# Kernel tuning notes

Measured on AMD Instinct MI355X. Metric: run time of the kernel, lower is better.

The kernel has to match this reference:

```python
import jax, jax.numpy as jnp
import numpy as np

# ---- hyperparameters (from init_kwargs) ----
SIGMA, RHO = 1.0, 10.0
ALPHA, BETA = 1.0, 1.0
K = 3  # ksize; patches are non-overlapping KxK, structure tensor computed on each patch
GRAY_W = np.array([0.2989, 0.587, 0.114], dtype=np.float32)  # torchvision Grayscale weights


def _gauss1d(sigma):
    d = np.arange(-1.0, 2.0, dtype=np.float32)  # radius-1 kernel (fits 3x3 patches)
    g = np.exp(-d * d / (2.0 * sigma * sigma))
    return (g / g.sum()).astype(np.float32)


def _dgauss1d(sigma):
    d = np.arange(-1.0, 2.0, dtype=np.float32)
    g = _gauss1d(sigma)
    return (-d / (sigma * sigma) * g).astype(np.float32)


def _conv3(x, k2d):
    # 'same' zero-padded 3x3 correlation over the last two dims, fully broadcast
    H, W = x.shape[-2], x.shape[-1]
    xp = jnp.pad(x, [(0, 0)] * (x.ndim - 2) + [(1, 1), (1, 1)])
    out = jnp.zeros_like(x)
    for i in range(3):
        for j in range(3):
            out = out + k2d[i, j] * xp[..., i:i + H, j:j + W]
    return out


# precomputed separable kernels (numpy constants)
_G_S, _DG_S, _G_R = _gauss1d(SIGMA), _dgauss1d(SIGMA), _gauss1d(RHO)
_KX = np.outer(_G_S, _DG_S)   # d/dx (last axis), gaussian-smoothed
_KY = np.outer(_DG_S, _G_S)   # d/dy
_KS = np.outer(_G_R, _G_R)    # rho smoothing


def _structure_tensor(gray):
    # gray: (..., K, K) -> (..., 3, K, K) components (Jxx, Jyy, Jxy)
    Ix = _conv3(gray, _KX)
    Iy = _conv3(gray, _KY)
    Jxx = _conv3(Ix * Ix, _KS)
    Jyy = _conv3(Iy * Iy, _KS)
    Jxy = _conv3(Ix * Iy, _KS)
    return jnp.stack([Jxx, Jyy, Jxy], axis=-3)


def _compute_patches(img):
    # img: (B, 3, H, W) -> (B, P, 3*K*K); non-overlapping KxK patches,
    # grayscale -> structure tensor -> per-patch L2 normalize (vectorized, no vmap-of-tiny-ops)
    B, C, H, W = img.shape
    Hb, Wb = H // K, W // K
    p = img.reshape(B, C, Hb, K, Wb, K).transpose(0, 2, 4, 1, 3, 5)  # (B,Hb,Wb,3,K,K)
    p = p.reshape(B, Hb * Wb, C, K, K)
    gray = jnp.einsum('bpchw,c->bphw', p, jnp.asarray(GRAY_W, p.dtype))
    st = _structure_tensor(gray)                                      # (B,P,3,K,K)
    n = jnp.sqrt(jnp.sum(st * st, axis=(-3, -2, -1), keepdims=True)) + 1e-12
    st = st / n
    return st.reshape(B, Hb * Wb, 3 * K * K)


def _resize(img, factor):
    B, C, H, W = img.shape
    return jax.image.resize(img, (B, C, int(H * factor), int(W * factor)),
                            method='bicubic', antialias=False)


def _pairdist_sq(a, b):
    # squared L2 pairwise distance (monotone in L2; only used for argmin)
    aa = jnp.sum(a * a, axis=-1)[:, :, None]
    bb = jnp.sum(b * b, axis=-1)[:, None, :]
    ab = jnp.einsum('bnw,bmw->bnm', a, b)
    return aa + bb - 2.0 * ab


def _loss(x, gt):
    p1 = _compute_patches(x)
    p2 = _compute_patches(gt)
    p2_2 = _compute_patches(_resize(gt, 0.5))
    p2_4 = _compute_patches(_resize(gt, 0.25))
    p2c = jnp.concatenate([p2, p2_2, p2_4], axis=1)      # (B, P2cat, 27)
    score = ALPHA * _pairdist_sq(p1, p2c) + BETA * _pairdist_sq(p2, p2c)
    ind = jnp.argmin(score, axis=2)                      # (B, P1) nearest-neighbor indices
    sel = jnp.take_along_axis(p2c, ind[:, :, None], axis=1)
    return jnp.mean(jnp.abs(p1 - sel))                   # L1 criterion


def setup_inputs() -> dict:
    key = jax.random.key(0)
    k1, k2 = jax.random.split(key)
    x = jax.random.uniform(k1, (4, 3, 192, 192), dtype=jnp.float32)
    gt = jax.random.uniform(k2, (4, 3, 192, 192), dtype=jnp.float32)
    return {'x': x, 'gt': gt}


def reference(x, gt):
    return _loss(x, gt)
```

## Files before the change

### kernel.cpp

```cpp
#include <hip/hip_runtime.h>
#include <hip/hip_bf16.h>
#include <math.h>

namespace {
constexpr int BATCH = 4;
constexpr int IMG   = 192;
constexpr int PL    = IMG * IMG;
constexpr int NP1   = 4096;
constexpr int N96   = 1024;
constexpr int N48   = 256;
constexpr int MALL  = 5376;
constexpr int RS    = 28;
constexpr int NCHUNK = 16;
constexpr int TPC    = 21;

#define GA 0.27406862f
#define GB 0.45186276f
#define RC 0.33277732f
#define RD 0.33444537f

typedef __bf16 bf16x8 __attribute__((ext_vector_type(8)));
typedef float  f32x4  __attribute__((ext_vector_type(4)));

__device__ __forceinline__ void conv3(const float in[9], const float k[9], float out[9]) {
#pragma unroll
  for (int y = 0; y < 3; ++y)
#pragma unroll
    for (int x = 0; x < 3; ++x) {
      float s = 0.f;
#pragma unroll
      for (int i = 0; i < 3; ++i) {
        int yy = y + i - 1;
        if (yy < 0 || yy > 2) continue;
#pragma unroll
        for (int j = 0; j < 3; ++j) {
          int xx = x + j - 1;
          if (xx < 0 || xx > 2) continue;
          s = fmaf(k[i * 3 + j], in[yy * 3 + xx], s);
        }
      }
      out[y * 3 + x] = s;
    }
}

__device__ __forceinline__ void st_from_gray(const float gray[9], float stv[27], float& cs) {
  const float KX[9] = {GA * GA, 0.f, -GA * GA, GB * GA, 0.f, -GB * GA, GA * GA, 0.f, -GA * GA};
  const float KY[9] = {GA * GA, GA * GB, GA * GA, 0.f, 0.f, 0.f, -GA * GA, -GA * GB, -GA * GA};
  const float KS[9] = {RC * RC, RC * RD, RC * RC, RD * RC, RD * RD, RD * RC, RC * RC, RC * RD, RC * RC};
  float Ix[9], Iy[9];
  conv3(gray, KX, Ix);
  conv3(gray, KY, Iy);
  float Pxx[9], Pyy[9], Pxy[9];
#pragma unroll
  for (int t = 0; t < 9; ++t) {
    Pxx[t] = Ix[t] * Ix[t];
    Pyy[t] = Iy[t] * Iy[t];
    Pxy[t] = Ix[t] * Iy[t];
  }
  conv3(Pxx, KS, stv + 0);
  conv3(Pyy, KS, stv + 9);
  conv3(Pxy, KS, stv + 18);
  float s2 = 0.f;
#pragma unroll
  for (int d = 0; d < 27; ++d) s2 = fmaf(stv[d], stv[d], s2);
  float inv = 1.0f / (sqrtf(s2) + 1e-12f);
  float c = 0.f;
#pragma unroll
  for (int d = 0; d < 27; ++d) {
    stv[d] *= inv;
    c = fmaf(stv[d], stv[d], c);
  }
  cs = c;
}

__device__ __forceinline__ void mkw(int k0, int IS, float w[4], int k[4]) {
  const float W4[4] = {-0.0625f, 0.5625f, 0.5625f, -0.0625f};
  float ssum = 0.f;
#pragma unroll
  for (int u = 0; u < 4; ++u) {
    int kk = k0 + u;
    bool v = (kk >= 0) && (kk < IS);
    w[u] = v ? W4[u] : 0.f;
    k[u] = v ? kk : 0;
    ssum += w[u];
  }
  float inv = 1.f / ssum;
#pragma unroll
  for (int u = 0; u < 4; ++u) w[u] *= inv;
}

__device__ __forceinline__ float bicubic_gray(const float* __restrict__ im,
                                              int i, int j, int step, int koff) {
  float wr[4], wc[4];
  int kr[4], kc[4];
  mkw(step * i + koff, IMG, wr, kr);
  mkw(step * j + koff, IMG, wc, kc);
  float acc = 0.f;
#pragma unroll
  for (int u = 0; u < 4; ++u) {
    float rs = 0.f;
#pragma unroll
    for (int v = 0; v < 4; ++v) {
      int o = kr[u] * IMG + kc[v];
      float r  = im[o];
      float g2 = im[PL + o];
      float bl = im[2 * PL + o];
      float gy = fmaf(0.114f, bl, fmaf(0.587f, g2, 0.2989f * r));
      rs = fmaf(wc[v], gy, rs);
    }
    acc = fmaf(wr[u], rs, acc);
  }
  return acc;
}

__device__ __forceinline__ void pack_row(const float v[28], unsigned* __restrict__ dst) {
  unsigned uh[16], ul[16];
#pragma unroll
  for (int p = 0; p < 16; ++p) {
    float a  = (2 * p < 28) ? v[2 * p] : 0.f;
    float bb = (2 * p + 1 < 28) ? v[2 * p + 1] : 0.f;
    __hip_bfloat16 ah = __float2bfloat16(a);
    __hip_bfloat16 bh = __float2bfloat16(bb);
    float af = __bfloat162float(ah), bf2 = __bfloat162float(bh);
    __hip_bfloat16 al = __float2bfloat16(a - af);
    __hip_bfloat16 bl = __float2bfloat16(bb - bf2);
    uh[p] = ((unsigned)__builtin_bit_cast(unsigned short, bh) << 16) |
            (unsigned)__builtin_bit_cast(unsigned short, ah);
    ul[p] = ((unsigned)__builtin_bit_cast(unsigned short, bl) << 16) |
            (unsigned)__builtin_bit_cast(unsigned short, al);
  }
  uint4* d4 = reinterpret_cast<uint4*>(dst);
  d4[0] = make_uint4(uh[0], uh[1], uh[2], uh[3]);
  d4[1] = make_uint4(uh[4], uh[5], uh[6], uh[7]);
  d4[2] = make_uint4(uh[8], uh[9], uh[10], uh[11]);
  d4[3] = make_uint4(uh[12], uh[13], uh[14], uh[15]);
  d4[4] = make_uint4(ul[0], ul[1], ul[2], ul[3]);
  d4[5] = make_uint4(ul[4], ul[5], ul[6], ul[7]);
  d4[6] = make_uint4(ul[8], ul[9], ul[10], ul[11]);
  d4[7] = make_uint4(ul[12], ul[13], ul[14], ul[15]);
}

__device__ __forceinline__ void store_row28(float* __restrict__ dst, const float v[28]) {
  float4* d4 = reinterpret_cast<float4*>(dst);
#pragma unroll
  for (int i = 0; i < 7; ++i)
    d4[i] = make_float4(v[4 * i], v[4 * i + 1], v[4 * i + 2], v[4 * i + 3]);
}

__global__ void __launch_bounds__(256) prep_kernel(
    const float* __restrict__ x, const float* __restrict__ gt,
    float* __restrict__ p1, float* __restrict__ p2c,
    unsigned* __restrict__ Qp, unsigned* __restrict__ Cp,
    unsigned* __restrict__ ctr) {
  int g = blockIdx.x * 256 + threadIdx.x;
  if (g == 0) ctr[0] = 0;

  if (g < BATCH * NP1) {
    int b = g >> 12, p = g & (NP1 - 1);
    int hb = p >> 6, wb = p & 63;
    const size_t boff = (size_t)b * 3 * PL + (size_t)(hb * 3) * IMG + wb * 3;

    float gr[9];
    const float* bx = x + boff;
#pragma unroll
    for (int y = 0; y < 3; ++y)
#pragma unroll
      for (int xx = 0; xx < 3; ++xx) {
        int o = y * IMG + xx;
        gr[y * 3 + xx] = fmaf(0.114f, bx[2 * PL + o], fmaf(0.587f, bx[PL + o], 0.2989f * bx[o]));
      }
    float s1[28];
    float cs1;
    st_from_gray(gr, s1, cs1);
    s1[27] = cs1;

    const float* bg = gt + boff;
#pragma unroll
    for (int y = 0; y < 3; ++y)
#pragma unroll
      for (int xx = 0; xx < 3; ++xx) {
        int o = y * IMG + xx;
        gr[y * 3 + xx] = fmaf(0.114f, bg[2 * PL + o], fmaf(0.587f, bg[PL + o], 0.2989f * bg[o]));
      }
    float s2[28];
    float cs2;
    st_from_gray(gr, s2, cs2);
    s2[27] = cs2;

    store_row28(p1 + (size_t)g * RS, s1);
    size_t crow = (size_t)b * MALL + p;
    store_row28(p2c + crow * RS, s2);

    float vc[28];
#pragma unroll
    for (int d = 0; d < 27; ++d) vc[d] = s2[d];
    vc[27] = -cs2;
    pack_row(vc, Cp + crow * 32);

    float vq[28];
#pragma unroll
    for (int d = 0; d < 27; ++d) vq[d] = s1[d] + s2[d];
    vq[27] = 1.0f;
    pack_row(vq, Qp + (size_t)g * 32);
  } else if (g < BATCH * (NP1 + N96)) {
    int q = g - BATCH * NP1;
    int b = q >> 10, p = q & (N96 - 1);
    int hb = p >> 5, wb = p & 31;
    const float* im = gt + (size_t)b * 3 * PL;
    float gr[9];
#pragma unroll
    for (int y = 0; y < 3; ++y)
#pragma unroll
      for (int xx = 0; xx < 3; ++xx)
        gr[y * 3 + xx] = bicubic_gray(im, 3 * hb + y, 3 * wb + xx, 2, -1);
    float s[28];
    float cs;
    st_from_gray(gr, s, cs);
    s[27] = cs;
    size_t crow = (size_t)b * MALL + NP1 + p;
    store_row28(p2c + crow * RS, s);
    float vc[28];
#pragma unroll
    for (int d = 0; d < 27; ++d) vc[d] = s[d];
    vc[27] = -cs;
    pack_row(vc, Cp + crow * 32);
  } else if (g < BATCH * (NP1 + N96 + N48)) {
    int q = g - BATCH * (NP1 + N96);
    int b = q >> 8, p = q & (N48 - 1);
    int hb = p >> 4, wb = p & 15;
    const float* im = gt + (size_t)b * 3 * PL;
    float gr[9];
#pragma unroll
    for (int y = 0; y < 3; ++y)
#pragma unroll
      for (int xx = 0; xx < 3; ++xx)
        gr[y * 3 + xx] = bicubic_gray(im, 3 * hb + y, 3 * wb + xx, 4, 0);
    float s[28];
    float cs;
    st_from_gray(gr, s, cs);
    s[27] = cs;
    size_t crow = (size_t)b * MALL + NP1 + N96 + p;
    store_row28(p2c + crow * RS, s);
    float vc[28];
#pragma unroll
    for (int d = 0; d < 27; ++d) vc[d] = s[d];
    vc[27] = -cs;
    pack_row(vc, Cp + crow * 32);
  }
}

__global__ void __launch_bounds__(256, 4) argmin_mfma_kernel(
    const unsigned* __restrict__ Qp, const unsigned* __restrict__ Cp,
    float* __restrict__ pscore, int* __restrict__ pidx) {
  const int lane = threadIdx.x & 63;
  const int w = threadIdx.x >> 6;
  const int chunk = blockIdx.y;
  const int b = blockIdx.z;
  const int nbase = blockIdx.x * 256 + w * 64;
  const int lm = lane & 15, lg = lane >> 4;

  bf16x8 qh[4], ql[4];
#pragma unroll
  for (int t = 0; t < 4; ++t) {
    const unsigned* rp = Qp + ((size_t)(b * NP1 + nbase + t * 16 + lm)) * 32 + lg * 4;
    qh[t] = *reinterpret_cast<const bf16x8*>(rp);
    ql[t] = *reinterpret_cast<const bf16x8*>(rp + 16);
  }

  float best[4][4];
  int idx[4][4];
#pragma unroll
  for (int t = 0; t < 4; ++t)
#pragma unroll
    for (int r = 0; r < 4; ++r) { best[t][r] = -INFINITY; idx[t][r] = 0; }

  const int tile0 = chunk * TPC;
  for (int i = 0; i < TPC; ++i) {
    const int m0 = (tile0 + i) * 16;
    const unsigned* cr = Cp + ((size_t)(b * MALL + m0 + lm)) * 32 + lg * 4;
    bf16x8 ch = *reinterpret_cast<const bf16x8*>(cr);
    bf16x8 cl = *reinterpret_cast<const bf16x8*>(cr + 16);
    const int mi = m0 + lm;
#pragma unroll
    for (int t = 0; t < 4; ++t) {
      f32x4 a = {0.f, 0.f, 0.f, 0.f};
      a = __builtin_amdgcn_mfma_f32_16x16x32_bf16(qh[t], ch, a, 0, 0, 0);
      a = __builtin_amdgcn_mfma_f32_16x16x32_bf16(ql[t], ch, a, 0, 0, 0);
      a = __builtin_amdgcn_mfma_f32_16x16x32_bf16(qh[t], cl, a, 0, 0, 0);
#pragma unroll
      for (int r = 0; r < 4; ++r) {
        bool g = a[r] > best[t][r];
        best[t][r] = g ? a[r] : best[t][r];
        idx[t][r] = g ? mi : idx[t][r];
      }
    }
  }

#pragma unroll
  for (int t = 0; t < 4; ++t)
#pragma unroll
    for (int r = 0; r < 4; ++r) {
      float bv = best[t][r];
      int bi = idx[t][r];
#pragma unroll
      for (int mk = 1; mk < 16; mk <<= 1) {
        float ov = __shfl_xor(bv, mk, 64);
        int oi = __shfl_xor(bi, mk, 64);
        bool take = (ov > bv) || (ov == bv && oi < bi);
        bv = take ? ov : bv;
        bi = take ? oi : bi;
      }
      if (lm == 0) {
        int row = nbase + t * 16 + lg * 4 + r;
        size_t o = ((size_t)(b * NP1 + row)) * NCHUNK + chunk;
        pscore[o] = bv;
        pidx[o] = bi;
      }
    }
}

__global__ void __launch_bounds__(256) finalize_kernel(
    const float* __restrict__ p1, const float* __restrict__ p2c,
    const float* __restrict__ pscore, const int* __restrict__ pidx,
    float* __restrict__ bsum, unsigned* __restrict__ ctr, float* __restrict__ out) {
  int g = blockIdx.x * 256 + threadIdx.x;
  float bt = -INFINITY;
  int bi = 0;
  for (int ms = 0; ms < NCHUNK; ++ms) {
    float s = pscore[(size_t)g * NCHUNK + ms];
    int ix = pidx[(size_t)g * NCHUNK + ms];
    bool gg = (s > bt) || (s == bt && ix < bi);
    bt = gg ? s : bt;
    bi = gg ? ix : bi;
  }
  int b = g >> 12;
  const float* a = p1 + (size_t)g * RS;
  const float* s2 = p2c + ((size_t)b * MALL + bi) * RS;
  float acc = 0.f;
#pragma unroll
  for (int d = 0; d < 27; ++d) acc += fabsf(a[d] - s2[d]);

  __shared__ float red[256];
  red[threadIdx.x] = acc;
  __syncthreads();
  for (int st = 128; st > 0; st >>= 1) {
    if (threadIdx.x < st) red[threadIdx.x] += red[threadIdx.x + st];
    __syncthreads();
  }
  if (threadIdx.x == 0) {
    __hip_atomic_store(&bsum[blockIdx.x], red[0], __ATOMIC_RELEASE, __HIP_MEMORY_SCOPE_AGENT);
    unsigned prev = __hip_atomic_fetch_add(ctr, 1u, __ATOMIC_ACQ_REL, __HIP_MEMORY_SCOPE_AGENT);
    if (prev == 63) {
      float s = 0.f;
      for (int i = 0; i < 64; ++i)
        s += __hip_atomic_load(&bsum[i], __ATOMIC_ACQUIRE, __HIP_MEMORY_SCOPE_AGENT);
      out[0] = s * (1.0f / 442368.0f);
    }
  }
}

}

extern "C" void kernel_launch(void* const* d_in, const int* in_sizes, int n_in,
                              void* d_out, int out_size, void* d_ws, size_t ws_size,
                              hipStream_t stream) {
  const float* x  = (const float*)d_in[0];
  const float* gt = (const float*)d_in[1];
  float* out = (float*)d_out;

  float* ws = (float*)d_ws;
  float* p1   = ws;
  float* p2c  = p1 + (size_t)BATCH * NP1 * RS;
  unsigned* Qp = (unsigned*)(p2c + (size_t)BATCH * MALL * RS);
  unsigned* Cp = Qp + (size_t)BATCH * NP1 * 32;
  float* pscore = (float*)(Cp + (size_t)BATCH * MALL * 32);
  int*   pidx   = (int*)(pscore + (size_t)BATCH * NP1 * NCHUNK);
  float* bsum   = (float*)(pidx + (size_t)BATCH * NP1 * NCHUNK);
  unsigned* ctr = (unsigned*)(bsum + 64);

  {
    int tot = BATCH * (NP1 + N96 + N48);
    prep_kernel<<<tot / 256, 256, 0, stream>>>(x, gt, p1, p2c, Qp, Cp, ctr);
  }

  {
    dim3 grid(16, NCHUNK, BATCH);
    argmin_mfma_kernel<<<grid, 256, 0, stream>>>(Qp, Cp, pscore, pidx);
  }

  finalize_kernel<<<(BATCH * NP1) / 256, 256, 0, stream>>>(p1, p2c, pscore, pidx, bsum, ctr, out);
}
```

Measured before the change: 74.75 us.

## Fragment-ordered packing, packed-key argmin, split prep, and chunk-count change

Stores the packed bf16 hi/lo rows for Q and C in MFMA fragment order, so each lane does one contiguous 16-byte load per operand. Prefetches the next C tile in the argmin loop and replaces the float-compare-plus-index tracking with a single unsigned max over keys whose low 5 bits hold a tile tag. Splits x and gt patch work across separate blocks, with a new small kernel building Q, and changes the chunking from 16x21 to 21x16 tiles. The key trick truncates 5 mantissa bits and offsets scores by +4 so they stay positive, which can change tie-breaking between near-equal candidates. It also adds an extra kernel launch.

```diff
diff --git a/kernel.cpp b/kernel.cpp
--- a/kernel.cpp
+++ b/kernel.cpp
@@ -7,12 +7,10 @@
 constexpr int IMG   = 192;
 constexpr int PL    = IMG * IMG;
 constexpr int NP1   = 4096;
-constexpr int N96   = 1024;
-constexpr int N48   = 256;
 constexpr int MALL  = 5376;
 constexpr int RS    = 28;
-constexpr int NCHUNK = 16;
-constexpr int TPC    = 21;
+constexpr int NCHUNK = 21;
+constexpr int TPC    = 16;
 
 #define GA 0.27406862f
 #define GB 0.45186276f
@@ -102,10 +100,7 @@
 #pragma unroll
     for (int v = 0; v < 4; ++v) {
       int o = kr[u] * IMG + kc[v];
-      float r  = im[o];
-      float g2 = im[PL + o];
-      float bl = im[2 * PL + o];
-      float gy = fmaf(0.114f, bl, fmaf(0.587f, g2, 0.2989f * r));
+      float gy = fmaf(0.114f, im[2 * PL + o], fmaf(0.587f, im[PL + o], 0.2989f * im[o]));
       rs = fmaf(wc[v], gy, rs);
     }
     acc = fmaf(wr[u], rs, acc);
@@ -113,12 +108,13 @@
   return acc;
 }
 
-__device__ __forceinline__ void pack_row(const float v[28], unsigned* __restrict__ dst) {
+__device__ __forceinline__ void pack_row_frag(const float* __restrict__ v, float tail,
+                                              unsigned* __restrict__ base, int rl) {
   unsigned uh[16], ul[16];
 #pragma unroll
   for (int p = 0; p < 16; ++p) {
-    float a  = (2 * p < 28) ? v[2 * p] : 0.f;
-    float bb = (2 * p + 1 < 28) ? v[2 * p + 1] : 0.f;
+    float a  = (2 * p < 27) ? v[2 * p] : 0.f;
+    float bb = (2 * p + 1 < 27) ? v[2 * p + 1] : (2 * p + 1 == 27 ? tail : 0.f);
     __hip_bfloat16 ah = __float2bfloat16(a);
     __hip_bfloat16 bh = __float2bfloat16(bb);
     float af = __bfloat162float(ah), bf2 = __bfloat162float(bh);
@@ -129,129 +125,106 @@
     ul[p] = ((unsigned)__builtin_bit_cast(unsigned short, bl) << 16) |
             (unsigned)__builtin_bit_cast(unsigned short, al);
   }
-  uint4* d4 = reinterpret_cast<uint4*>(dst);
-  d4[0] = make_uint4(uh[0], uh[1], uh[2], uh[3]);
-  d4[1] = make_uint4(uh[4], uh[5], uh[6], uh[7]);
-  d4[2] = make_uint4(uh[8], uh[9], uh[10], uh[11]);
-  d4[3] = make_uint4(uh[12], uh[13], uh[14], uh[15]);
-  d4[4] = make_uint4(ul[0], ul[1], ul[2], ul[3]);
-  d4[5] = make_uint4(ul[4], ul[5], ul[6], ul[7]);
-  d4[6] = make_uint4(ul[8], ul[9], ul[10], ul[11]);
-  d4[7] = make_uint4(ul[12], ul[13], ul[14], ul[15]);
-}
-
-__device__ __forceinline__ void store_row28(float* __restrict__ dst, const float v[28]) {
+#pragma unroll
+  for (int lg = 0; lg < 4; ++lg) {
+    *reinterpret_cast<uint4*>(base + (size_t)(lg * 16 + rl) * 4) =
+        make_uint4(uh[4 * lg], uh[4 * lg + 1], uh[4 * lg + 2], uh[4 * lg + 3]);
+    *reinterpret_cast<uint4*>(base + 256 + (size_t)(lg * 16 + rl) * 4) =
+        make_uint4(ul[4 * lg], ul[4 * lg + 1], ul[4 * lg + 2], ul[4 * lg + 3]);
+  }
+}
+
+__device__ __forceinline__ void store_row28(float* __restrict__ dst, const float v[27], float tail) {
   float4* d4 = reinterpret_cast<float4*>(dst);
 #pragma unroll
-  for (int i = 0; i < 7; ++i)
+  for (int i = 0; i < 6; ++i)
     d4[i] = make_float4(v[4 * i], v[4 * i + 1], v[4 * i + 2], v[4 * i + 3]);
-}
-
-__global__ void __launch_bounds__(256) prep_kernel(
+  d4[6] = make_float4(v[24], v[25], v[26], tail);
+}
+
+__global__ void __launch_bounds__(256) prep_all_kernel(
     const float* __restrict__ x, const float* __restrict__ gt,
     float* __restrict__ p1, float* __restrict__ p2c,
-    unsigned* __restrict__ Qp, unsigned* __restrict__ Cp,
-    unsigned* __restrict__ ctr) {
-  int g = blockIdx.x * 256 + threadIdx.x;
-  if (g == 0) ctr[0] = 0;
-
-  if (g < BATCH * NP1) {
-    int b = g >> 12, p = g & (NP1 - 1);
-    int hb = p >> 6, wb = p & 63;
-    const size_t boff = (size_t)b * 3 * PL + (size_t)(hb * 3) * IMG + wb * 3;
-
+    unsigned* __restrict__ Cp, unsigned* __restrict__ ctr) {
+  const int bid = blockIdx.x;
+  const int t = threadIdx.x;
+  if (bid == 0 && t == 0) ctr[0] = 0;
+
+  if (bid < 128) {
+    const bool isx = bid < 64;
+    const int gid = (isx ? bid : bid - 64) * 256 + t;
+    const int b = gid >> 12, p = gid & (NP1 - 1);
+    const int hb = p >> 6, wb = p & 63;
+    const float* base = (isx ? x : gt) + (size_t)b * 3 * PL + (size_t)(hb * 3) * IMG + wb * 3;
     float gr[9];
-    const float* bx = x + boff;
 #pragma unroll
     for (int y = 0; y < 3; ++y)
 #pragma unroll
       for (int xx = 0; xx < 3; ++xx) {
         int o = y * IMG + xx;
-        gr[y * 3 + xx] = fmaf(0.114f, bx[2 * PL + o], fmaf(0.587f, bx[PL + o], 0.2989f * bx[o]));
-      }
-    float s1[28];
-    float cs1;
-    st_from_gray(gr, s1, cs1);
-    s1[27] = cs1;
-
-    const float* bg = gt + boff;
-#pragma unroll
-    for (int y = 0; y < 3; ++y)
-#pragma unroll
-      for (int xx = 0; xx < 3; ++xx) {
-        int o = y * IMG + xx;
-        gr[y * 3 + xx] = fmaf(0.114f, bg[2 * PL + o], fmaf(0.587f, bg[PL + o], 0.2989f * bg[o]));
-      }
-    float s2[28];
-    float cs2;
-    st_from_gray(gr, s2, cs2);
-    s2[27] = cs2;
-
-    store_row28(p1 + (size_t)g * RS, s1);
-    size_t crow = (size_t)b * MALL + p;
-    store_row28(p2c + crow * RS, s2);
-
-    float vc[28];
-#pragma unroll
-    for (int d = 0; d < 27; ++d) vc[d] = s2[d];
-    vc[27] = -cs2;
-    pack_row(vc, Cp + crow * 32);
-
-    float vq[28];
-#pragma unroll
-    for (int d = 0; d < 27; ++d) vq[d] = s1[d] + s2[d];
-    vq[27] = 1.0f;
-    pack_row(vq, Qp + (size_t)g * 32);
-  } else if (g < BATCH * (NP1 + N96)) {
-    int q = g - BATCH * NP1;
-    int b = q >> 10, p = q & (N96 - 1);
-    int hb = p >> 5, wb = p & 31;
-    const float* im = gt + (size_t)b * 3 * PL;
-    float gr[9];
-#pragma unroll
-    for (int y = 0; y < 3; ++y)
-#pragma unroll
-      for (int xx = 0; xx < 3; ++xx)
-        gr[y * 3 + xx] = bicubic_gray(im, 3 * hb + y, 3 * wb + xx, 2, -1);
-    float s[28];
+        gr[y * 3 + xx] = fmaf(0.114f, base[2 * PL + o],
+                              fmaf(0.587f, base[PL + o], 0.2989f * base[o]));
+      }
+    float s[27];
     float cs;
     st_from_gray(gr, s, cs);
-    s[27] = cs;
-    size_t crow = (size_t)b * MALL + NP1 + p;
-    store_row28(p2c + crow * RS, s);
-    float vc[28];
-#pragma unroll
-    for (int d = 0; d < 27; ++d) vc[d] = s[d];
-    vc[27] = -cs;
-    pack_row(vc, Cp + crow * 32);
-  } else if (g < BATCH * (NP1 + N96 + N48)) {
-    int q = g - BATCH * (NP1 + N96);
-    int b = q >> 8, p = q & (N48 - 1);
-    int hb = p >> 4, wb = p & 15;
-    const float* im = gt + (size_t)b * 3 * PL;
+    if (isx) {
+      store_row28(p1 + (size_t)gid * RS, s, cs);
+    } else {
+      size_t crow = (size_t)b * MALL + p;
+      store_row28(p2c + crow * RS, s, cs);
+      pack_row_frag(s, -cs, Cp + (crow >> 4) * 512, (int)(crow & 15));
+    }
+  } else {
+    int row;
     float gr[9];
-#pragma unroll
-    for (int y = 0; y < 3; ++y)
-#pragma unroll
-      for (int xx = 0; xx < 3; ++xx)
-        gr[y * 3 + xx] = bicubic_gray(im, 3 * hb + y, 3 * wb + xx, 4, 0);
-    float s[28];
+    if (bid < 144) {
+      int q = (bid - 128) * 256 + t;
+      int b = q >> 10, p = q & 1023;
+      int hb = p >> 5, wb = p & 31;
+      const float* im = gt + (size_t)b * 3 * PL;
+#pragma unroll
+      for (int y = 0; y < 3; ++y)
+#pragma unroll
+        for (int xx = 0; xx < 3; ++xx)
+          gr[y * 3 + xx] = bicubic_gray(im, 3 * hb + y, 3 * wb + xx, 2, -1);
+      row = b * MALL + NP1 + p;
+    } else {
+      int q = (bid - 144) * 256 + t;
+      int b = q >> 8, p = q & 255;
+      int hb = p >> 4, wb = p & 15;
+      const float* im = gt + (size_t)b * 3 * PL;
+#pragma unroll
+      for (int y = 0; y < 3; ++y)
+#pragma unroll
+        for (int xx = 0; xx < 3; ++xx)
+          gr[y * 3 + xx] = bicubic_gray(im, 3 * hb + y, 3 * wb + xx, 4, 0);
+      row = b * MALL + NP1 + 1024 + p;
+    }
+    float s[27];
     float cs;
     st_from_gray(gr, s, cs);
-    s[27] = cs;
-    size_t crow = (size_t)b * MALL + NP1 + N96 + p;
-    store_row28(p2c + crow * RS, s);
-    float vc[28];
-#pragma unroll
-    for (int d = 0; d < 27; ++d) vc[d] = s[d];
-    vc[27] = -cs;
-    pack_row(vc, Cp + crow * 32);
-  }
+    store_row28(p2c + (size_t)row * RS, s, cs);
+    pack_row_frag(s, -cs, Cp + ((size_t)row >> 4) * 512, row & 15);
+  }
+}
+
+__global__ void __launch_bounds__(256) pack_q_kernel(
+    const float* __restrict__ p1, const float* __restrict__ p2c,
+    unsigned* __restrict__ Qp) {
+  int gid = blockIdx.x * 256 + threadIdx.x;
+  int b = gid >> 12, n = gid & (NP1 - 1);
+  const float* a = p1 + (size_t)gid * RS;
+  const float* c = p2c + ((size_t)b * MALL + n) * RS;
+  float v[27];
+#pragma unroll
+  for (int d = 0; d < 27; ++d) v[d] = a[d] + c[d];
+  pack_row_frag(v, 1.0f, Qp + (size_t)(gid >> 4) * 512, gid & 15);
 }
 
 __global__ void __launch_bounds__(256, 4) argmin_mfma_kernel(
     const unsigned* __restrict__ Qp, const unsigned* __restrict__ Cp,
-    float* __restrict__ pscore, int* __restrict__ pidx) {
+    unsigned* __restrict__ pkey, int* __restrict__ pidx) {
   const int lane = threadIdx.x & 63;
   const int w = threadIdx.x >> 6;
   const int chunk = blockIdx.y;
@@ -262,75 +235,77 @@
   bf16x8 qh[4], ql[4];
 #pragma unroll
   for (int t = 0; t < 4; ++t) {
-    const unsigned* rp = Qp + ((size_t)(b * NP1 + nbase + t * 16 + lm)) * 32 + lg * 4;
-    qh[t] = *reinterpret_cast<const bf16x8*>(rp);
-    ql[t] = *reinterpret_cast<const bf16x8*>(rp + 16);
-  }
-
-  float best[4][4];
-  int idx[4][4];
+    const unsigned* tb = Qp + (size_t)((b * NP1 + nbase) >> 4) * 512 + (size_t)t * 512 + lane * 4;
+    qh[t] = *reinterpret_cast<const bf16x8*>(tb);
+    ql[t] = *reinterpret_cast<const bf16x8*>(tb + 256);
+  }
+
+  unsigned keys[4][4];
 #pragma unroll
   for (int t = 0; t < 4; ++t)
 #pragma unroll
-    for (int r = 0; r < 4; ++r) { best[t][r] = -INFINITY; idx[t][r] = 0; }
+    for (int r = 0; r < 4; ++r) keys[t][r] = 0u;
 
   const int tile0 = chunk * TPC;
+  const unsigned* cb = Cp + (size_t)(b * (MALL >> 4) + tile0) * 512 + lane * 4;
+  bf16x8 ch = *reinterpret_cast<const bf16x8*>(cb);
+  bf16x8 cl = *reinterpret_cast<const bf16x8*>(cb + 256);
   for (int i = 0; i < TPC; ++i) {
-    const int m0 = (tile0 + i) * 16;
-    const unsigned* cr = Cp + ((size_t)(b * MALL + m0 + lm)) * 32 + lg * 4;
-    bf16x8 ch = *reinterpret_cast<const bf16x8*>(cr);
-    bf16x8 cl = *reinterpret_cast<const bf16x8*>(cr + 16);
-    const int mi = m0 + lm;
+    cb += 512;
+    bf16x8 nh = *reinterpret_cast<const bf16x8*>(cb);
+    bf16x8 nl = *reinterpret_cast<const bf16x8*>(cb + 256);
+    const unsigned tag = (unsigned)(TPC - 1 - i);
 #pragma unroll
     for (int t = 0; t < 4; ++t) {
-      f32x4 a = {0.f, 0.f, 0.f, 0.f};
+      f32x4 a = {4.f, 4.f, 4.f, 4.f};
       a = __builtin_amdgcn_mfma_f32_16x16x32_bf16(qh[t], ch, a, 0, 0, 0);
       a = __builtin_amdgcn_mfma_f32_16x16x32_bf16(ql[t], ch, a, 0, 0, 0);
       a = __builtin_amdgcn_mfma_f32_16x16x32_bf16(qh[t], cl, a, 0, 0, 0);
 #pragma unroll
       for (int r = 0; r < 4; ++r) {
-        bool g = a[r] > best[t][r];
-        best[t][r] = g ? a[r] : best[t][r];
-        idx[t][r] = g ? mi : idx[t][r];
-      }
-    }
+        unsigned kb = (__builtin_bit_cast(unsigned, (float)a[r]) & 0xFFFFFFE0u) | tag;
+        keys[t][r] = keys[t][r] > kb ? keys[t][r] : kb;
+      }
+    }
+    ch = nh;
+    cl = nl;
   }
 
 #pragma unroll
   for (int t = 0; t < 4; ++t)
 #pragma unroll
     for (int r = 0; r < 4; ++r) {
-      float bv = best[t][r];
-      int bi = idx[t][r];
+      unsigned k = keys[t][r];
+      int m = (tile0 + (int)((unsigned)(TPC - 1) - (k & 31u))) * 16 + lm;
 #pragma unroll
       for (int mk = 1; mk < 16; mk <<= 1) {
-        float ov = __shfl_xor(bv, mk, 64);
-        int oi = __shfl_xor(bi, mk, 64);
-        bool take = (ov > bv) || (ov == bv && oi < bi);
-        bv = take ? ov : bv;
-        bi = take ? oi : bi;
+        unsigned ok = (unsigned)__shfl_xor((int)k, mk, 64);
+        int om = __shfl_xor(m, mk, 64);
+        bool take = (ok > k) || (ok == k && om < m);
+        k = take ? ok : k;
+        m = take ? om : m;
       }
       if (lm == 0) {
         int row = nbase + t * 16 + lg * 4 + r;
         size_t o = ((size_t)(b * NP1 + row)) * NCHUNK + chunk;
-        pscore[o] = bv;
-        pidx[o] = bi;
+        pkey[o] = k & 0xFFFFFFE0u;
+        pidx[o] = m;
       }
     }
 }
 
 __global__ void __launch_bounds__(256) finalize_kernel(
     const float* __restrict__ p1, const float* __restrict__ p2c,
-    const float* __restrict__ pscore, const int* __restrict__ pidx,
+    const unsigned* __restrict__ pkey, const int* __restrict__ pidx,
     float* __restrict__ bsum, unsigned* __restrict__ ctr, float* __restrict__ out) {
   int g = blockIdx.x * 256 + threadIdx.x;
-  float bt = -INFINITY;
+  unsigned bk = 0u;
   int bi = 0;
   for (int ms = 0; ms < NCHUNK; ++ms) {
-    float s = pscore[(size_t)g * NCHUNK + ms];
+    unsigned k = pkey[(size_t)g * NCHUNK + ms];
     int ix = pidx[(size_t)g * NCHUNK + ms];
-    bool gg = (s > bt) || (s == bt && ix < bi);
-    bt = gg ? s : bt;
+    bool gg = k > bk;
+    bk = gg ? k : bk;
     bi = gg ? ix : bi;
   }
   int b = g >> 12;
@@ -373,20 +348,19 @@
   float* p2c  = p1 + (size_t)BATCH * NP1 * RS;
   unsigned* Qp = (unsigned*)(p2c + (size_t)BATCH * MALL * RS);
   unsigned* Cp = Qp + (size_t)BATCH * NP1 * 32;
-  float* pscore = (float*)(Cp + (size_t)BATCH * MALL * 32);
-  int*   pidx   = (int*)(pscore + (size_t)BATCH * NP1 * NCHUNK);
+  unsigned* pkey = Cp + (size_t)BATCH * MALL * 32 + 512;
+  int*   pidx   = (int*)(pkey + (size_t)BATCH * NP1 * NCHUNK);
   float* bsum   = (float*)(pidx + (size_t)BATCH * NP1 * NCHUNK);
   unsigned* ctr = (unsigned*)(bsum + 64);
 
-  {
-    int tot = BATCH * (NP1 + N96 + N48);
-    prep_kernel<<<tot / 256, 256, 0, stream>>>(x, gt, p1, p2c, Qp, Cp, ctr);
-  }
+  prep_all_kernel<<<148, 256, 0, stream>>>(x, gt, p1, p2c, Cp, ctr);
+
+  pack_q_kernel<<<64, 256, 0, stream>>>(p1, p2c, Qp);
 
   {
     dim3 grid(16, NCHUNK, BATCH);
-    argmin_mfma_kernel<<<grid, 256, 0, stream>>>(Qp, Cp, pscore, pidx);
-  }
-
-  finalize_kernel<<<(BATCH * NP1) / 256, 256, 0, stream>>>(p1, p2c, pscore, pidx, bsum, ctr, out);
-}
+    argmin_mfma_kernel<<<grid, 256, 0, stream>>>(Qp, Cp, pkey, pidx);
+  }
+
+  finalize_kernel<<<64, 256, 0, stream>>>(p1, p2c, pkey, pidx, bsum, ctr, out);
+}
```

Result: slower. 170.6 us (+128.2%).
